# Kernel tuning notes

Measured on AMD Instinct MI355X. Metric: run time of the kernel, lower is better.

## Reference

```python
import jax, jax.numpy as jnp
import numpy as np

H, N_PATCH, F, DIM = 12, 196, 8, 768
DH = DIM // H            # 64
D3 = 3 * DH              # per-head dim after 3*dim projection = 192
SCALE = float(np.sqrt(DH) * H)
B, S = 8, 1 + N_PATCH * F  # 1569


def setup_inputs() -> dict:
    key = jax.random.key(0)
    ks = jax.random.split(key, 12)
    w = lambda k, shp: (jax.random.normal(k, shp, dtype=jnp.float32) * 0.02)
    return {
        "x": jax.random.normal(ks[0], (B, S, DIM), dtype=jnp.float32),
        "Wq": w(ks[1], (DIM, 3 * DIM)), "bq": jnp.zeros((3 * DIM,), jnp.float32),
        "Wk": w(ks[2], (DIM, 3 * DIM)), "bk": jnp.zeros((3 * DIM,), jnp.float32),
        "Wv": w(ks[3], (DIM, 3 * DIM)), "bv": jnp.zeros((3 * DIM,), jnp.float32),
        "Wt": w(ks[4], (3 * DIM, DIM)), "bt": jnp.zeros((DIM,), jnp.float32),
        "Wf": w(ks[5], (3 * DIM, DIM)), "bf": jnp.zeros((DIM,), jnp.float32),
    }


def _heads(t):
    # [b, s, 3*dim] -> [b, H, s, D3]
    b, s, _ = t.shape
    return t.reshape(b, s, H, D3).transpose(0, 2, 1, 3)


def _merge(t):
    # [b, H, s, D3] -> [b, s, 3*dim]
    b, _, s, _ = t.shape
    return t.transpose(0, 2, 1, 3).reshape(b, s, H * D3)


def _attn(q, k, v):
    a = jax.nn.softmax(jnp.einsum('bhqd,bhkd->bhqk', q, k) / SCALE, axis=-1)
    return jnp.einsum('bhqk,bhkd->bhqd', a, v)


def reference(x, Wq, bq, Wk, bk, Wv, bv, Wt, bt, Wf, bf):
    patches = x[:, 1:, :]                       # [b, n*F, dim]
    # NOTE: faithful to original code: v_mat comes from self.k, k_mat from self.v
    qm = _heads(patches @ Wq + bq)
    vm = _heads(patches @ Wk + bk)
    km = _heads(patches @ Wv + bv)

    # CLS attention over full sequence (here v from self.v, k from self.k)
    q_cls = _heads(x[:, 0:1, :] @ Wq + bq)      # [b,H,1,D3]
    v_cls = _heads(x @ Wv + bv)
    k_cls = _heads(x @ Wk + bk)
    inter_cls = _attn(q_cls, k_cls, v_cls)      # [b,H,1,D3]

    # Stage 1: temporal attention per patch (patches 1..n-1), vectorized.
    # tokens are frame-major: index = frame*n + patch, so slice p::n == patch p across frames
    def per_patch(t):
        b = t.shape[0]
        return t.reshape(b, H, F, N_PATCH, D3)[:, :, :, 1:, :].transpose(0, 1, 3, 2, 4)  # [b,H,n-1,F,D3]
    q5, k5, v5 = per_patch(qm), per_patch(km), per_patch(vm)
    a1 = jax.nn.softmax(jnp.einsum('bhpfd,bhpgd->bhpfg', q5, k5) / SCALE, axis=-1)
    t1 = jnp.einsum('bhpfg,bhpgd->bhpfd', a1, v5).sum(axis=3)   # [b,H,n-1,D3]
    t1 = jnp.tile(t1, (1, 1, F, 1))                              # [b,H,(n-1)*F,D3]
    ti = _merge(t1) @ Wt + bt                                    # [b,(n-1)*F,dim]

    # Stage 2 (same qkv swap as stage 1)
    q2 = _heads(ti @ Wq + bq)
    v2 = _heads(ti @ Wk + bk)
    k2 = _heads(ti @ Wv + bv)
    outs = [_attn(q2[:, :, 0:N_PATCH], k2[:, :, 0:N_PATCH], v2[:, :, 0:N_PATCH]).sum(axis=2, keepdims=True)]
    for xi in range(1, F):  # small fixed loop over num_frames
        o = _attn(q2[:, :, xi:xi + N_PATCH], k2[:, :, xi::N_PATCH], v2[:, :, xi::N_PATCH])
        outs.append(o.sum(axis=2, keepdims=True))
    t2 = jnp.concatenate(outs, axis=2)                           # [b,H,F,D3]
    t2 = jnp.tile(t2, (1, 1, N_PATCH, 1))                        # [b,H,F*n,D3]

    full = jnp.concatenate([inter_cls, t2], axis=2)              # [b,H,1+n*F,D3]
    return _merge(full) @ Wf + bf                                # [b,S,dim]
```

## Files before the change

kernel.cpp:

```cpp
#include <hip/hip_runtime.h>
#include <math.h>

#define B_    8
#define SEQ   1569
#define DIMX  768
#define H_    12
#define D3    192
#define F_    8
#define NP    196
#define P1    195
#define NCOL  2304
#define NS    6912
#define RSCALE (1.0f/96.0f)
#define NCHUNK 16
#define CH     99
#define CLS_STRIDE 196

typedef __bf16 bf16_t;
typedef bf16_t bf16x8 __attribute__((ext_vector_type(8)));
typedef float  f32x4  __attribute__((ext_vector_type(4)));

__device__ __forceinline__ void load_lds16(const bf16_t* g, bf16_t* l) {
  __builtin_amdgcn_global_load_lds(
      (const __attribute__((address_space(1))) void*)g,
      (__attribute__((address_space(3))) void*)l, 16, 0, 0);
}

__device__ __forceinline__ float block_max256(float v, float* red) {
  #pragma unroll
  for (int o = 32; o > 0; o >>= 1) v = fmaxf(v, __shfl_xor(v, o, 64));
  __syncthreads();
  if ((threadIdx.x & 63) == 0) red[threadIdx.x >> 6] = v;
  __syncthreads();
  return fmaxf(fmaxf(red[0], red[1]), fmaxf(red[2], red[3]));
}

__device__ __forceinline__ float block_sum256(float v, float* red) {
  #pragma unroll
  for (int o = 32; o > 0; o >>= 1) v += __shfl_xor(v, o, 64);
  __syncthreads();
  if ((threadIdx.x & 63) == 0) red[threadIdx.x >> 6] = v;
  __syncthreads();
  return red[0] + red[1] + red[2] + red[3];
}

__global__ __launch_bounds__(256) void cast_f32_bf16(
    const float* __restrict__ in, bf16_t* __restrict__ out, int n4) {
  const int i = blockIdx.x * 256 + threadIdx.x;
  if (i >= n4) return;
  const float4 v = ((const float4*)in)[i];
  bf16_t o4[4] = {(bf16_t)v.x, (bf16_t)v.y, (bf16_t)v.z, (bf16_t)v.w};
  ((uint2*)out)[i] = *(uint2*)o4;
}

__global__ __launch_bounds__(256) void concat_bias_kernel(
    const float* __restrict__ bq, const float* __restrict__ bk,
    const float* __restrict__ bv, float* __restrict__ qkvb) {
  const int i = blockIdx.x * 256 + threadIdx.x;
  if (i >= NS) return;
  float v;
  if (i < NCOL) v = bq[i];
  else if (i < 2 * NCOL) v = bk[i - NCOL];
  else v = bv[i - 2 * NCOL];
  qkvb[i] = v;
}

__global__ __launch_bounds__(256) void transpose_cast(
    const float* __restrict__ W, bf16_t* __restrict__ WT, int Kd, int Nd) {
  __shared__ float t[32][33];
  const int bn = blockIdx.x * 32;
  const int bk = blockIdx.y * 32;
  const int tx = threadIdx.x & 31, ty = threadIdx.x >> 5;
  #pragma unroll
  for (int i = 0; i < 32; i += 8)
    t[ty + i][tx] = W[(size_t)(bk + ty + i) * Nd + bn + tx];
  __syncthreads();
  #pragma unroll
  for (int i = 0; i < 32; i += 8)
    WT[(size_t)(bn + ty + i) * Kd + bk + tx] = (bf16_t)t[tx][ty + i];
}

__global__ __launch_bounds__(256) void gemm_mfma_bt(
    const bf16_t* __restrict__ A, const bf16_t* __restrict__ BT,
    const float* __restrict__ bias, void* __restrict__ C,
    int M, int N, int K, int MT, int NT, int GROUPM, int outBf16) {
  __shared__ bf16_t As[128 * 32];
  __shared__ bf16_t Bs[128 * 32];
  const int tid  = threadIdx.x;
  const int wave = tid >> 6, lane = tid & 63;

  const int pid   = blockIdx.x;
  const int npg   = GROUPM * NT;
  const int group = pid / npg;
  const int first_m = group * GROUPM;
  int gsm = MT - first_m; if (gsm > GROUPM) gsm = GROUPM;
  const int lpid  = pid % npg;
  const int m_tile = first_m + lpid % gsm;
  const int n_tile = lpid / gsm;
  const int row0 = m_tile * 128, col0 = n_tile * 128;

  const int fr = lane & 15, kg = lane >> 4;
  int ra0 = row0 + wave * 32 + fr;
  int ra1 = ra0 + 16;
  if (ra0 >= M) ra0 = M - 1;
  if (ra1 >= M) ra1 = M - 1;
  const bf16_t* Ap0 = A + (size_t)ra0 * K + kg * 8;
  const bf16_t* Ap1 = A + (size_t)ra1 * K + kg * 8;
  const bf16_t* Bp0 = BT + (size_t)(col0 + wave * 32 + fr) * K + kg * 8;
  const bf16_t* Bp1 = Bp0 + (size_t)16 * K;
  bf16_t* lA0 = &As[(wave * 2 + 0) * 512];
  bf16_t* lA1 = &As[(wave * 2 + 1) * 512];
  bf16_t* lB0 = &Bs[(wave * 2 + 0) * 512];
  bf16_t* lB1 = &Bs[(wave * 2 + 1) * 512];

  const int m0 = (wave & 1) * 64, n0 = (wave >> 1) * 64;
  const int mb = (wave & 1) * 4,  nb = (wave >> 1) * 4;
  f32x4 acc[4][4] = {};

  for (int k0 = 0; k0 < K; k0 += 32) {
    load_lds16(Ap0 + k0, lA0);
    load_lds16(Ap1 + k0, lA1);
    load_lds16(Bp0 + k0, lB0);
    load_lds16(Bp1 + k0, lB1);
    __syncthreads();

    bf16x8 af[4], bfr[4];
    #pragma unroll
    for (int i = 0; i < 4; ++i) {
      af[i]  = *(const bf16x8*)&As[(mb + i) * 512 + lane * 8];
      bfr[i] = *(const bf16x8*)&Bs[(nb + i) * 512 + lane * 8];
    }
    #pragma unroll
    for (int i = 0; i < 4; ++i)
      #pragma unroll
      for (int j = 0; j < 4; ++j)
        acc[i][j] = __builtin_amdgcn_mfma_f32_16x16x32_bf16(
            af[i], bfr[j], acc[i][j], 0, 0, 0);
    __syncthreads();
  }

  const int cc = lane & 15, cr4 = (lane >> 4) * 4;
  #pragma unroll
  for (int i = 0; i < 4; ++i) {
    #pragma unroll
    for (int j = 0; j < 4; ++j) {
      const int col = col0 + n0 + j * 16 + cc;
      const float bcol = bias[col];
      #pragma unroll
      for (int reg = 0; reg < 4; ++reg) {
        const int r = row0 + m0 + i * 16 + cr4 + reg;
        if (r < M) {
          const float v = acc[i][j][reg] + bcol;
          if (outBf16) ((bf16_t*)C)[(size_t)r * N + col] = (bf16_t)v;
          else         ((float*)C)[(size_t)r * N + col] = v;
        }
      }
    }
  }
}

__global__ __launch_bounds__(256) void xi0_scores_mfma(
    const bf16_t* __restrict__ QKV2, float* __restrict__ Smat) {
  __shared__ bf16_t As[128 * 32];
  __shared__ bf16_t Bs[128 * 32];
  const int tid  = threadIdx.x;
  const int wave = tid >> 6, lane = tid & 63;
  const int row0 = blockIdx.x * 128, col0 = blockIdx.y * 128;
  const int bh = blockIdx.z;
  const int b = bh / H_, h = bh % H_;
  const bf16_t* Abase = QKV2 + (size_t)b * P1 * NS + h * D3;
  const bf16_t* Bbase = QKV2 + (size_t)b * P1 * NS + 2 * NCOL + h * D3;

  const int fr = lane & 15, kg = lane >> 4;
  int ra0 = row0 + wave * 32 + fr;
  int ra1 = ra0 + 16;
  if (ra0 >= P1) ra0 = P1 - 1;
  if (ra1 >= P1) ra1 = P1 - 1;
  int cb0 = col0 + wave * 32 + fr;
  int cb1 = cb0 + 16;
  if (cb0 >= P1) cb0 = P1 - 1;
  if (cb1 >= P1) cb1 = P1 - 1;
  const bf16_t* Ap0 = Abase + (size_t)ra0 * NS + kg * 8;
  const bf16_t* Ap1 = Abase + (size_t)ra1 * NS + kg * 8;
  const bf16_t* Bp0 = Bbase + (size_t)cb0 * NS + kg * 8;
  const bf16_t* Bp1 = Bbase + (size_t)cb1 * NS + kg * 8;
  bf16_t* lA0 = &As[(wave * 2 + 0) * 512];
  bf16_t* lA1 = &As[(wave * 2 + 1) * 512];
  bf16_t* lB0 = &Bs[(wave * 2 + 0) * 512];
  bf16_t* lB1 = &Bs[(wave * 2 + 1) * 512];

  const int m0 = (wave & 1) * 64, n0 = (wave >> 1) * 64;
  const int mb = (wave & 1) * 4,  nb = (wave >> 1) * 4;
  f32x4 acc[4][4] = {};

  for (int k0 = 0; k0 < D3; k0 += 32) {
    load_lds16(Ap0 + k0, lA0);
    load_lds16(Ap1 + k0, lA1);
    load_lds16(Bp0 + k0, lB0);
    load_lds16(Bp1 + k0, lB1);
    __syncthreads();
    bf16x8 af[4], bfr[4];
    #pragma unroll
    for (int i = 0; i < 4; ++i) {
      af[i]  = *(const bf16x8*)&As[(mb + i) * 512 + lane * 8];
      bfr[i] = *(const bf16x8*)&Bs[(nb + i) * 512 + lane * 8];
    }
    #pragma unroll
    for (int i = 0; i < 4; ++i)
      #pragma unroll
      for (int j = 0; j < 4; ++j)
        acc[i][j] = __builtin_amdgcn_mfma_f32_16x16x32_bf16(
            af[i], bfr[j], acc[i][j], 0, 0, 0);
    __syncthreads();
  }

  float* S = Smat + (size_t)bh * P1 * P1;
  const int cc = lane & 15, cr4 = (lane >> 4) * 4;
  #pragma unroll
  for (int i = 0; i < 4; ++i)
    #pragma unroll
    for (int j = 0; j < 4; ++j) {
      const int col = col0 + n0 + j * 16 + cc;
      #pragma unroll
      for (int reg = 0; reg < 4; ++reg) {
        const int r = row0 + m0 + i * 16 + cr4 + reg;
        if (r < P1 && col < P1) S[(size_t)r * P1 + col] = acc[i][j][reg] * RSCALE;
      }
    }
}

__global__ __launch_bounds__(256) void xi0_finish_kernel(
    const float* __restrict__ Smat, const bf16_t* __restrict__ QKV2,
    bf16_t* __restrict__ FULL9b) {
  const int bh = blockIdx.x;
  const int b = bh / H_, h = bh % H_;
  __shared__ float mrow[P1], inv_l[P1], g[P1];
  const float* S = Smat + (size_t)bh * P1 * P1;
  const int tid = threadIdx.x;

  if (tid < P1) {
    float m = -1e30f;
    for (int k = 0; k < P1; ++k) m = fmaxf(m, S[(size_t)tid * P1 + k]);
    float l = 0.f;
    for (int k = 0; k < P1; ++k)
      l += expf(S[(size_t)tid * P1 + k] - m) * ((k == 0) ? 2.f : 1.f);
    mrow[tid] = m;
    inv_l[tid] = ((tid == 0) ? 2.f : 1.f) / l;
  }
  __syncthreads();
  if (tid < P1) {
    float s = 0.f;
    for (int r = 0; r < P1; ++r)
      s += expf(S[(size_t)r * P1 + tid] - mrow[r]) * inv_l[r];
    g[tid] = s * ((tid == 0) ? 2.f : 1.f);
  }
  __syncthreads();
  if (tid < D3) {
    float acc = 0.f;
    const bf16_t* vbase = QKV2 + (size_t)b * P1 * NS + NCOL + h * D3 + tid;
    for (int k = 0; k < P1; ++k)
      acc = fmaf(g[k], (float)vbase[(size_t)k * NS], acc);
    FULL9b[((size_t)b * 9 + 1) * NCOL + h * D3 + tid] = (bf16_t)acc;
  }
}

__global__ __launch_bounds__(256) void cls_part_kernel(
    const bf16_t* __restrict__ XQKV, float* __restrict__ CLSP, int b0) {
  const int h  = blockIdx.x % H_;
  const int bl = blockIdx.x / H_;
  const int b  = b0 + bl;
  const int c  = blockIdx.y;
  const int t0 = c * CH;
  const int tend = (t0 + CH < SEQ) ? t0 + CH : SEQ;
  __shared__ float qs[D3];
  __shared__ float sc[CH];
  __shared__ float red[4];
  const int tid = threadIdx.x;

  const bf16_t* Qr = XQKV + (size_t)bl * SEQ * NS + h * D3;
  if (tid < 24) {
    const bf16x8 q8 = *(const bf16x8*)(Qr + tid * 8);
    #pragma unroll
    for (int m2 = 0; m2 < 8; ++m2) qs[tid * 8 + m2] = (float)q8[m2];
  }
  __syncthreads();

  float lmax = -1e30f;
  for (int t = t0 + tid; t < tend; t += 256) {
    const bf16_t* kr = XQKV + ((size_t)bl * SEQ + t) * NS + NCOL + h * D3;
    float acc = 0.f;
    #pragma unroll 3
    for (int d = 0; d < D3; d += 8) {
      const bf16x8 k8 = *(const bf16x8*)(kr + d);
      #pragma unroll
      for (int m2 = 0; m2 < 8; ++m2) acc = fmaf(qs[d + m2], (float)k8[m2], acc);
    }
    acc *= RSCALE;
    sc[t - t0] = acc;
    lmax = fmaxf(lmax, acc);
  }
  const float m = block_max256(lmax, red);
  float lsum = 0.f;
  for (int t = t0 + tid; t < tend; t += 256) {
    const float e = expf(sc[t - t0] - m);
    sc[t - t0] = e;
    lsum += e;
  }
  const float L = block_sum256(lsum, red);
  __syncthreads();

  float* P = CLSP + ((size_t)(b * H_ + h) * NCHUNK + c) * CLS_STRIDE;
  if (tid < D3) {
    float acc = 0.f;
    const bf16_t* vbase = XQKV + ((size_t)bl * SEQ + t0) * NS + 2 * NCOL + h * D3 + tid;
    for (int t = t0; t < tend; ++t)
      acc = fmaf(sc[t - t0], (float)vbase[(size_t)(t - t0) * NS], acc);
    P[tid] = acc;
  }
  if (tid == 192) P[192] = m;
  if (tid == 193) P[193] = L;
}

__global__ __launch_bounds__(256) void cls_combine_kernel(
    const float* __restrict__ CLSP, bf16_t* __restrict__ FULL9b) {
  const int bh = blockIdx.x;
  const int tid = threadIdx.x;
  const float* P = CLSP + (size_t)bh * NCHUNK * CLS_STRIDE;

  float M = -1e30f;
  #pragma unroll
  for (int c = 0; c < NCHUNK; ++c) M = fmaxf(M, P[c * CLS_STRIDE + 192]);
  float L = 0.f;
  float w[NCHUNK];
  #pragma unroll
  for (int c = 0; c < NCHUNK; ++c) {
    w[c] = expf(P[c * CLS_STRIDE + 192] - M);
    L += P[c * CLS_STRIDE + 193] * w[c];
  }
  if (tid < D3) {
    float acc = 0.f;
    #pragma unroll
    for (int c = 0; c < NCHUNK; ++c)
      acc = fmaf(w[c], P[c * CLS_STRIDE + tid], acc);
    const int b = bh / H_, h = bh % H_;
    FULL9b[((size_t)b * 9 + 0) * NCOL + h * D3 + tid] = (bf16_t)(acc / L);
  }
}

__global__ __launch_bounds__(64) void temporal_kernel(
    const bf16_t* __restrict__ XQKV, bf16_t* __restrict__ T1U, int b0) {
  const int id = blockIdx.x;
  const int pi = id % P1;
  const int h  = (id / P1) % H_;
  const int bl = id / (P1 * H_);
  const int b  = b0 + bl;
  __shared__ float qs[8][196], ks[8][196];
  const int tid = threadIdx.x;

  #pragma unroll
  for (int i = 0; i < 6; ++i) {
    const int idx = tid + 64 * i;
    const int arr = idx / 192;
    const int c = idx % 192;
    const int f = c / 24, d0 = (c % 24) * 8;
    const size_t base = ((size_t)bl * SEQ + (size_t)f * NP + pi + 2) * NS +
                        (arr ? 2 * NCOL : 0) + h * D3 + d0;
    const bf16x8 v8 = *(const bf16x8*)(XQKV + base);
    float* dst = arr ? &ks[f][d0] : &qs[f][d0];
    #pragma unroll
    for (int m2 = 0; m2 < 8; ++m2) dst[m2] = (float)v8[m2];
  }
  __syncthreads();

  const int f = tid >> 3, g = tid & 7;
  float s = 0.f;
  for (int d = 0; d < D3; d += 4) {
    const float4 a4 = *(const float4*)&qs[f][d];
    const float4 b4 = *(const float4*)&ks[g][d];
    s = fmaf(a4.x, b4.x, s); s = fmaf(a4.y, b4.y, s);
    s = fmaf(a4.z, b4.z, s); s = fmaf(a4.w, b4.w, s);
  }
  s *= RSCALE;

  float m = s;
  #pragma unroll
  for (int o = 1; o < 8; o <<= 1) m = fmaxf(m, __shfl_xor(m, o, 64));
  const float e = expf(s - m);
  float sum = e;
  #pragma unroll
  for (int o = 1; o < 8; o <<= 1) sum += __shfl_xor(sum, o, 64);
  float a = e / sum;
  #pragma unroll
  for (int o = 8; o < 64; o <<= 1) a += __shfl_xor(a, o, 64);
  float wg[8];
  #pragma unroll
  for (int gg = 0; gg < 8; ++gg) wg[gg] = __shfl(a, gg, 64);

  const size_t vrow = (size_t)bl * SEQ * NS + NCOL + h * D3;
  #pragma unroll
  for (int i = 0; i < 3; ++i) {
    const int d = tid + 64 * i;
    float o = 0.f;
    #pragma unroll
    for (int gg = 0; gg < 8; ++gg) {
      const bf16_t vv = XQKV[vrow + ((size_t)gg * NP + pi + 2) * NS + d];
      o = fmaf(wg[gg], (float)vv, o);
    }
    T1U[((size_t)b * P1 + pi) * NCOL + h * D3 + d] = (bf16_t)o;
  }
}

__global__ __launch_bounds__(256) void stage2_xi_kernel(
    const bf16_t* __restrict__ QKV2, bf16_t* __restrict__ FULL9b) {
  const int xi = 1 + blockIdx.x % 7;
  const int h  = (blockIdx.x / 7) % H_;
  const int b  = blockIdx.x / (7 * H_);
  __shared__ float Ks[8][196], Vs[8][196], Qs[32][196];
  __shared__ float Pp[32][8];
  const int tid = threadIdx.x;

  for (int idx = tid; idx < 192; idx += 256) {
    const int k = idx / 24, d0 = (idx % 24) * 8;
    const bf16x8 v8 = *(const bf16x8*)(QKV2 + ((size_t)(b * P1 + xi + k)) * NS +
                                       2 * NCOL + h * D3 + d0);
    #pragma unroll
    for (int m2 = 0; m2 < 8; ++m2) Ks[k][d0 + m2] = (float)v8[m2];
  }
  for (int idx = tid; idx < 192; idx += 256) {
    const int k = idx / 24, d0 = (idx % 24) * 8;
    const bf16x8 v8 = *(const bf16x8*)(QKV2 + ((size_t)(b * P1 + xi + k)) * NS +
                                       NCOL + h * D3 + d0);
    #pragma unroll
    for (int m2 = 0; m2 < 8; ++m2) Vs[k][d0 + m2] = (float)v8[m2];
  }

  float acc = 0.f;
  for (int c = 0; c < 7; ++c) {
    __syncthreads();
    for (int idx = tid; idx < 768; idx += 256) {
      const int qr = idx / 24, d0 = (idx % 24) * 8;
      const int rq = c * 32 + qr;
      if (rq < P1) {
        const bf16x8 v8 = *(const bf16x8*)(QKV2 + ((size_t)(b * P1 + rq)) * NS +
                                           h * D3 + d0);
        #pragma unroll
        for (int m2 = 0; m2 < 8; ++m2) Qs[qr][d0 + m2] = (float)v8[m2];
      } else {
        #pragma unroll
        for (int m2 = 0; m2 < 8; ++m2) Qs[qr][d0 + m2] = 0.f;
      }
    }
    __syncthreads();
    const int grp = tid >> 3, k = tid & 7;
    float dot = 0.f;
    for (int d = 0; d < D3; d += 4) {
      const float4 a4 = *(const float4*)&Qs[grp][d];
      const float4 b4 = *(const float4*)&Ks[k][d];
      dot = fmaf(a4.x, b4.x, dot); dot = fmaf(a4.y, b4.y, dot);
      dot = fmaf(a4.z, b4.z, dot); dot = fmaf(a4.w, b4.w, dot);
    }
    dot *= RSCALE;
    float m = dot;
    #pragma unroll
    for (int o = 1; o < 8; o <<= 1) m = fmaxf(m, __shfl_xor(m, o, 64));
    const float e = expf(dot - m);
    float s = e;
    #pragma unroll
    for (int o = 1; o < 8; o <<= 1) s += __shfl_xor(s, o, 64);
    Pp[grp][k] = e / s;
    __syncthreads();
    if (tid < D3) {
      #pragma unroll 4
      for (int g2 = 0; g2 < 32; ++g2) {
        const int rq2 = c * 32 + g2;
        if (rq2 < P1) {
          const float mult = (rq2 == xi) ? 2.f : 1.f;
          float o = 0.f;
          #pragma unroll
          for (int kk = 0; kk < 8; ++kk) o = fmaf(Pp[g2][kk], Vs[kk][tid], o);
          acc = fmaf(mult, o, acc);
        }
      }
    }
  }
  if (tid < D3)
    FULL9b[((size_t)b * 9 + 1 + xi) * NCOL + h * D3 + tid] = (bf16_t)acc;
}

__global__ __launch_bounds__(256) void bcast_kernel(
    const float* __restrict__ OUT9, float* __restrict__ out) {
  const int idx = blockIdx.x * 256 + threadIdx.x;
  const int total = B_ * SEQ * (DIMX / 4);
  if (idx >= total) return;
  const int d4 = idx % (DIMX / 4);
  const int bs = idx / (DIMX / 4);
  const int s = bs % SEQ;
  const int b = bs / SEQ;
  const int row = (s == 0) ? 0 : 1 + ((s - 1) & 7);
  ((float4*)out)[idx] = ((const float4*)OUT9)[(size_t)(b * 9 + row) * (DIMX / 4) + d4];
}

extern "C" void kernel_launch(void* const* d_in, const int* in_sizes, int n_in,
                              void* d_out, int out_size, void* d_ws, size_t ws_size,
                              hipStream_t stream) {
  const float* x  = (const float*)d_in[0];
  const float* Wq = (const float*)d_in[1];
  const float* bq = (const float*)d_in[2];
  const float* Wk = (const float*)d_in[3];
  const float* bk = (const float*)d_in[4];
  const float* Wv = (const float*)d_in[5];
  const float* bv = (const float*)d_in[6];
  const float* Wt = (const float*)d_in[7];
  const float* bt = (const float*)d_in[8];
  const float* Wf = (const float*)d_in[9];
  const float* bf = (const float*)d_in[10];
  float* out = (float*)d_out;
  (void)in_sizes; (void)n_in; (void)out_size;

  char* ws = (char*)d_ws;
  size_t off = 0;
  auto alloc_f32 = [&](size_t elems) {
    size_t a = (off + 63) & ~(size_t)63;
    off = a + elems * sizeof(float);
    return (float*)(ws + a);
  };
  auto alloc_bf16 = [&](size_t elems) {
    size_t a = (off + 63) & ~(size_t)63;
    off = a + elems * sizeof(bf16_t);
    return (bf16_t*)(ws + a);
  };

  bf16_t* T1Ub   = alloc_bf16((size_t)B_ * P1 * NCOL);
  bf16_t* TIUb   = alloc_bf16((size_t)B_ * P1 * DIMX);
  bf16_t* QKV2b  = alloc_bf16((size_t)B_ * P1 * NS);
  bf16_t* FULL9b = alloc_bf16((size_t)B_ * 9 * NCOL);
  float*  OUT9   = alloc_f32((size_t)B_ * 9 * DIMX);
  float*  Smat   = alloc_f32((size_t)B_ * H_ * P1 * P1);
  float*  CLSP   = alloc_f32((size_t)B_ * H_ * NCHUNK * CLS_STRIDE);
  float*  QKVbias= alloc_f32(NS);
  bf16_t* WqkvT  = alloc_bf16((size_t)3 * NCOL * DIMX);
  bf16_t* WtT    = alloc_bf16((size_t)DIMX * NCOL);
  bf16_t* WfT    = alloc_bf16((size_t)DIMX * NCOL);

  const size_t remain = (ws_size > off) ? (ws_size - off) : 0;
  int Bc = 8;
  while (Bc > 1 &&
         (size_t)Bc * SEQ * (NS + DIMX) * sizeof(bf16_t) + 512 > remain)
    Bc >>= 1;
  bf16_t* XQKVb = alloc_bf16((size_t)Bc * SEQ * NS);
  bf16_t* xb    = alloc_bf16((size_t)Bc * SEQ * DIMX);

  transpose_cast<<<dim3(NCOL / 32, DIMX / 32), 256, 0, stream>>>(
      Wq, WqkvT + 0 * (size_t)NCOL * DIMX, DIMX, NCOL);
  transpose_cast<<<dim3(NCOL / 32, DIMX / 32), 256, 0, stream>>>(
      Wk, WqkvT + 1 * (size_t)NCOL * DIMX, DIMX, NCOL);
  transpose_cast<<<dim3(NCOL / 32, DIMX / 32), 256, 0, stream>>>(
      Wv, WqkvT + 2 * (size_t)NCOL * DIMX, DIMX, NCOL);
  transpose_cast<<<dim3(DIMX / 32, NCOL / 32), 256, 0, stream>>>(Wt, WtT, NCOL, DIMX);
  transpose_cast<<<dim3(DIMX / 32, NCOL / 32), 256, 0, stream>>>(Wf, WfT, NCOL, DIMX);
  concat_bias_kernel<<<dim3((NS + 255) / 256), 256, 0, stream>>>(bq, bk, bv, QKVbias);

  for (int b0 = 0; b0 < B_; b0 += Bc) {
    const int Mrows = Bc * SEQ;
    const int n4 = Mrows * DIMX / 4;
    cast_f32_bf16<<<dim3((n4 + 255) / 256), 256, 0, stream>>>(
        x + (size_t)b0 * SEQ * DIMX, xb, n4);
    const int MT = (Mrows + 127) / 128, NT = NS / 128;
    gemm_mfma_bt<<<dim3(MT * NT), 256, 0, stream>>>(
        xb, WqkvT, QKVbias, XQKVb, Mrows, NS, DIMX, MT, NT, 8, 1);
    cls_part_kernel<<<dim3(Bc * H_, NCHUNK), 256, 0, stream>>>(XQKVb, CLSP, b0);
    temporal_kernel<<<dim3(Bc * P1 * H_), 64, 0, stream>>>(XQKVb, T1Ub, b0);
  }
  cls_combine_kernel<<<dim3(B_ * H_), 256, 0, stream>>>(CLSP, FULL9b);

  {
    const int MT = (B_ * P1 + 127) / 128, NT = DIMX / 128;
    gemm_mfma_bt<<<dim3(MT * NT), 256, 0, stream>>>(
        T1Ub, WtT, bt, TIUb, B_ * P1, DIMX, NCOL, MT, NT, 4, 1);
  }
  {
    const int MT = (B_ * P1 + 127) / 128, NT = NS / 128;
    gemm_mfma_bt<<<dim3(MT * NT), 256, 0, stream>>>(
        TIUb, WqkvT, QKVbias, QKV2b, B_ * P1, NS, DIMX, MT, NT, 4, 1);
  }

  xi0_scores_mfma<<<dim3(2, 2, B_ * H_), 256, 0, stream>>>(QKV2b, Smat);
  xi0_finish_kernel<<<dim3(B_ * H_), 256, 0, stream>>>(Smat, QKV2b, FULL9b);
  stage2_xi_kernel<<<dim3(B_ * H_ * 7), 256, 0, stream>>>(QKV2b, FULL9b);

  {
    const int MT = 1, NT = DIMX / 128;
    gemm_mfma_bt<<<dim3(MT * NT), 256, 0, stream>>>(
        FULL9b, WfT, bf, OUT9, B_ * 9, DIMX, NCOL, MT, NT, 1, 0);
  }

  {
    const int total4 = B_ * SEQ * (DIMX / 4);
    bcast_kernel<<<dim3((total4 + 255) / 256), 256, 0, stream>>>(OUT9, out);
  }
}
```

Baseline: 834.7 us.

## Double-buffer GEMM LDS, XCD-aware tile mapping, batch temporal blocks, fuse weight transposes

The GEMM now double-buffers its A/B LDS tiles and prefetches the next K slice before computing the current one, using explicit waitcnt and barriers in place of full syncthreads. The big QKV GEMM gets an XCD-aware block-to-tile mapping so each of the 8 XCDs works on a contiguous band of M tiles, aiming at better L2 reuse. The temporal kernel packs four patches into one 256-thread block instead of one patch per 64-thread block. The five weight transpose launches are merged into one kernel. Risks are hand-coded waitcnt encodings being wrong for the target, LDS use doubling and lowering occupancy, and some wasted idle blocks in the XCD mapping.

```diff
diff --git a/kernel.cpp b/kernel.cpp
--- a/kernel.cpp
+++ b/kernel.cpp
@@ -15,6 +15,7 @@
 #define NCHUNK 16
 #define CH     99
 #define CLS_STRIDE 196
+#define PG4   49
 
 typedef __bf16 bf16_t;
 typedef bf16_t bf16x8 __attribute__((ext_vector_type(8)));
@@ -65,11 +66,27 @@
   qkvb[i] = v;
 }
 
-__global__ __launch_bounds__(256) void transpose_cast(
-    const float* __restrict__ W, bf16_t* __restrict__ WT, int Kd, int Nd) {
+__global__ __launch_bounds__(256) void transpose_all(
+    const float* __restrict__ Wq, const float* __restrict__ Wk,
+    const float* __restrict__ Wv, const float* __restrict__ Wt,
+    const float* __restrict__ Wf, bf16_t* __restrict__ WqkvT,
+    bf16_t* __restrict__ WtT, bf16_t* __restrict__ WfT) {
   __shared__ float t[32][33];
-  const int bn = blockIdx.x * 32;
-  const int bk = blockIdx.y * 32;
+  const int bid = blockIdx.x;
+  const int mat = bid / 1728, tt = bid % 1728;
+  const float* W; bf16_t* WT; int Kd, Nd, nt, kt;
+  if (mat < 3) {
+    Kd = DIMX; Nd = NCOL;
+    W = (mat == 0) ? Wq : ((mat == 1) ? Wk : Wv);
+    WT = WqkvT + (size_t)mat * NCOL * DIMX;
+    nt = tt % 72; kt = tt / 72;
+  } else {
+    Kd = NCOL; Nd = DIMX;
+    W = (mat == 3) ? Wt : Wf;
+    WT = (mat == 3) ? WtT : WfT;
+    nt = tt % 24; kt = tt / 24;
+  }
+  const int bn = nt * 32, bk = kt * 32;
   const int tx = threadIdx.x & 31, ty = threadIdx.x >> 5;
   #pragma unroll
   for (int i = 0; i < 32; i += 8)
@@ -83,20 +100,28 @@
 __global__ __launch_bounds__(256) void gemm_mfma_bt(
     const bf16_t* __restrict__ A, const bf16_t* __restrict__ BT,
     const float* __restrict__ bias, void* __restrict__ C,
-    int M, int N, int K, int MT, int NT, int GROUPM, int outBf16) {
-  __shared__ bf16_t As[128 * 32];
-  __shared__ bf16_t Bs[128 * 32];
+    int M, int N, int K, int MT, int NT, int GROUPM, int XCDB, int outBf16) {
+  __shared__ bf16_t As[2][128 * 32];
+  __shared__ bf16_t Bs[2][128 * 32];
   const int tid  = threadIdx.x;
   const int wave = tid >> 6, lane = tid & 63;
 
-  const int pid   = blockIdx.x;
-  const int npg   = GROUPM * NT;
-  const int group = pid / npg;
-  const int first_m = group * GROUPM;
-  int gsm = MT - first_m; if (gsm > GROUPM) gsm = GROUPM;
-  const int lpid  = pid % npg;
-  const int m_tile = first_m + lpid % gsm;
-  const int n_tile = lpid / gsm;
+  int m_tile, n_tile;
+  const int pid = blockIdx.x;
+  if (XCDB > 0) {
+    const int xcd = pid & 7, q = pid >> 3;
+    m_tile = xcd * XCDB + q % XCDB;
+    n_tile = q / XCDB;
+    if (m_tile >= MT) return;
+  } else {
+    const int npg   = GROUPM * NT;
+    const int group = pid / npg;
+    const int first_m = group * GROUPM;
+    int gsm = MT - first_m; if (gsm > GROUPM) gsm = GROUPM;
+    const int lpid  = pid % npg;
+    m_tile = first_m + lpid % gsm;
+    n_tile = lpid / gsm;
+  }
   const int row0 = m_tile * 128, col0 = n_tile * 128;
 
   const int fr = lane & 15, kg = lane >> 4;
@@ -108,27 +133,37 @@
   const bf16_t* Ap1 = A + (size_t)ra1 * K + kg * 8;
   const bf16_t* Bp0 = BT + (size_t)(col0 + wave * 32 + fr) * K + kg * 8;
   const bf16_t* Bp1 = Bp0 + (size_t)16 * K;
-  bf16_t* lA0 = &As[(wave * 2 + 0) * 512];
-  bf16_t* lA1 = &As[(wave * 2 + 1) * 512];
-  bf16_t* lB0 = &Bs[(wave * 2 + 0) * 512];
-  bf16_t* lB1 = &Bs[(wave * 2 + 1) * 512];
+  const int la0 = (wave * 2 + 0) * 512, la1 = (wave * 2 + 1) * 512;
 
   const int m0 = (wave & 1) * 64, n0 = (wave >> 1) * 64;
   const int mb = (wave & 1) * 4,  nb = (wave >> 1) * 4;
   f32x4 acc[4][4] = {};
 
-  for (int k0 = 0; k0 < K; k0 += 32) {
-    load_lds16(Ap0 + k0, lA0);
-    load_lds16(Ap1 + k0, lA1);
-    load_lds16(Bp0 + k0, lB0);
-    load_lds16(Bp1 + k0, lB1);
-    __syncthreads();
+  const int nk = K >> 5;
+  load_lds16(Ap0, &As[0][la0]);
+  load_lds16(Ap1, &As[0][la1]);
+  load_lds16(Bp0, &Bs[0][la0]);
+  load_lds16(Bp1, &Bs[0][la1]);
+
+  for (int kk = 0; kk < nk; ++kk) {
+    const int p = kk & 1;
+    if (kk + 1 < nk) {
+      const int k0 = (kk + 1) * 32;
+      load_lds16(Ap0 + k0, &As[p ^ 1][la0]);
+      load_lds16(Ap1 + k0, &As[p ^ 1][la1]);
+      load_lds16(Bp0 + k0, &Bs[p ^ 1][la0]);
+      load_lds16(Bp1 + k0, &Bs[p ^ 1][la1]);
+      __builtin_amdgcn_s_waitcnt(0x0F74);
+    } else {
+      __builtin_amdgcn_s_waitcnt(0x0F70);
+    }
+    __builtin_amdgcn_s_barrier();
 
     bf16x8 af[4], bfr[4];
     #pragma unroll
     for (int i = 0; i < 4; ++i) {
-      af[i]  = *(const bf16x8*)&As[(mb + i) * 512 + lane * 8];
-      bfr[i] = *(const bf16x8*)&Bs[(nb + i) * 512 + lane * 8];
+      af[i]  = *(const bf16x8*)&As[p][(mb + i) * 512 + lane * 8];
+      bfr[i] = *(const bf16x8*)&Bs[p][(nb + i) * 512 + lane * 8];
     }
     #pragma unroll
     for (int i = 0; i < 4; ++i)
@@ -136,7 +171,7 @@
       for (int j = 0; j < 4; ++j)
         acc[i][j] = __builtin_amdgcn_mfma_f32_16x16x32_bf16(
             af[i], bfr[j], acc[i][j], 0, 0, 0);
-    __syncthreads();
+    __builtin_amdgcn_s_barrier();
   }
 
   const int cc = lane & 15, cr4 = (lane >> 4) * 4;
@@ -347,36 +382,40 @@
   }
 }
 
-__global__ __launch_bounds__(64) void temporal_kernel(
+__global__ __launch_bounds__(256) void temporal_kernel(
     const bf16_t* __restrict__ XQKV, bf16_t* __restrict__ T1U, int b0) {
   const int id = blockIdx.x;
-  const int pi = id % P1;
-  const int h  = (id / P1) % H_;
-  const int bl = id / (P1 * H_);
+  const int pg = id % PG4;
+  const int h  = (id / PG4) % H_;
+  const int bl = id / (PG4 * H_);
   const int b  = b0 + bl;
-  __shared__ float qs[8][196], ks[8][196];
-  const int tid = threadIdx.x;
+  const int wave = threadIdx.x >> 6, lane = threadIdx.x & 63;
+  __shared__ float qs[4][8][196], ks[4][8][196];
+
+  int pi = pg * 4 + wave;
+  const bool act = (pi < P1);
+  if (!act) pi = P1 - 1;
 
   #pragma unroll
   for (int i = 0; i < 6; ++i) {
-    const int idx = tid + 64 * i;
+    const int idx = lane + 64 * i;
     const int arr = idx / 192;
     const int c = idx % 192;
     const int f = c / 24, d0 = (c % 24) * 8;
     const size_t base = ((size_t)bl * SEQ + (size_t)f * NP + pi + 2) * NS +
                         (arr ? 2 * NCOL : 0) + h * D3 + d0;
     const bf16x8 v8 = *(const bf16x8*)(XQKV + base);
-    float* dst = arr ? &ks[f][d0] : &qs[f][d0];
+    float* dst = arr ? &ks[wave][f][d0] : &qs[wave][f][d0];
     #pragma unroll
     for (int m2 = 0; m2 < 8; ++m2) dst[m2] = (float)v8[m2];
   }
   __syncthreads();
 
-  const int f = tid >> 3, g = tid & 7;
+  const int f = lane >> 3, g = lane & 7;
   float s = 0.f;
   for (int d = 0; d < D3; d += 4) {
-    const float4 a4 = *(const float4*)&qs[f][d];
-    const float4 b4 = *(const float4*)&ks[g][d];
+    const float4 a4 = *(const float4*)&qs[wave][f][d];
+    const float4 b4 = *(const float4*)&ks[wave][g][d];
     s = fmaf(a4.x, b4.x, s); s = fmaf(a4.y, b4.y, s);
     s = fmaf(a4.z, b4.z, s); s = fmaf(a4.w, b4.w, s);
   }
@@ -396,17 +435,19 @@
   #pragma unroll
   for (int gg = 0; gg < 8; ++gg) wg[gg] = __shfl(a, gg, 64);
 
-  const size_t vrow = (size_t)bl * SEQ * NS + NCOL + h * D3;
-  #pragma unroll
-  for (int i = 0; i < 3; ++i) {
-    const int d = tid + 64 * i;
-    float o = 0.f;
-    #pragma unroll
-    for (int gg = 0; gg < 8; ++gg) {
-      const bf16_t vv = XQKV[vrow + ((size_t)gg * NP + pi + 2) * NS + d];
-      o = fmaf(wg[gg], (float)vv, o);
-    }
-    T1U[((size_t)b * P1 + pi) * NCOL + h * D3 + d] = (bf16_t)o;
+  if (act) {
+    const size_t vrow = (size_t)bl * SEQ * NS + NCOL + h * D3;
+    #pragma unroll
+    for (int i = 0; i < 3; ++i) {
+      const int d = lane + 64 * i;
+      float o = 0.f;
+      #pragma unroll
+      for (int gg = 0; gg < 8; ++gg) {
+        const bf16_t vv = XQKV[vrow + ((size_t)gg * NP + pi + 2) * NS + d];
+        o = fmaf(wg[gg], (float)vv, o);
+      }
+      T1U[((size_t)b * P1 + pi) * NCOL + h * D3 + d] = (bf16_t)o;
+    }
   }
 }
 
@@ -550,14 +591,8 @@
   bf16_t* XQKVb = alloc_bf16((size_t)Bc * SEQ * NS);
   bf16_t* xb    = alloc_bf16((size_t)Bc * SEQ * DIMX);
 
-  transpose_cast<<<dim3(NCOL / 32, DIMX / 32), 256, 0, stream>>>(
-      Wq, WqkvT + 0 * (size_t)NCOL * DIMX, DIMX, NCOL);
-  transpose_cast<<<dim3(NCOL / 32, DIMX / 32), 256, 0, stream>>>(
-      Wk, WqkvT + 1 * (size_t)NCOL * DIMX, DIMX, NCOL);
-  transpose_cast<<<dim3(NCOL / 32, DIMX / 32), 256, 0, stream>>>(
-      Wv, WqkvT + 2 * (size_t)NCOL * DIMX, DIMX, NCOL);
-  transpose_cast<<<dim3(DIMX / 32, NCOL / 32), 256, 0, stream>>>(Wt, WtT, NCOL, DIMX);
-  transpose_cast<<<dim3(DIMX / 32, NCOL / 32), 256, 0, stream>>>(Wf, WfT, NCOL, DIMX);
+  transpose_all<<<dim3(1728 * 5), 256, 0, stream>>>(
+      Wq, Wk, Wv, Wt, Wf, WqkvT, WtT, WfT);
   concat_bias_kernel<<<dim3((NS + 255) / 256), 256, 0, stream>>>(bq, bk, bv, QKVbias);
 
   for (int b0 = 0; b0 < B_; b0 += Bc) {
@@ -566,22 +601,23 @@
     cast_f32_bf16<<<dim3((n4 + 255) / 256), 256, 0, stream>>>(
         x + (size_t)b0 * SEQ * DIMX, xb, n4);
     const int MT = (Mrows + 127) / 128, NT = NS / 128;
-    gemm_mfma_bt<<<dim3(MT * NT), 256, 0, stream>>>(
-        xb, WqkvT, QKVbias, XQKVb, Mrows, NS, DIMX, MT, NT, 8, 1);
+    const int XCDB = (MT + 7) / 8;
+    gemm_mfma_bt<<<dim3(8 * XCDB * NT), 256, 0, stream>>>(
+        xb, WqkvT, QKVbias, XQKVb, Mrows, NS, DIMX, MT, NT, 0, XCDB, 1);
     cls_part_kernel<<<dim3(Bc * H_, NCHUNK), 256, 0, stream>>>(XQKVb, CLSP, b0);
-    temporal_kernel<<<dim3(Bc * P1 * H_), 64, 0, stream>>>(XQKVb, T1Ub, b0);
+    temporal_kernel<<<dim3(Bc * H_ * PG4), 256, 0, stream>>>(XQKVb, T1Ub, b0);
   }
   cls_combine_kernel<<<dim3(B_ * H_), 256, 0, stream>>>(CLSP, FULL9b);
 
   {
     const int MT = (B_ * P1 + 127) / 128, NT = DIMX / 128;
     gemm_mfma_bt<<<dim3(MT * NT), 256, 0, stream>>>(
-        T1Ub, WtT, bt, TIUb, B_ * P1, DIMX, NCOL, MT, NT, 4, 1);
+        T1Ub, WtT, bt, TIUb, B_ * P1, DIMX, NCOL, MT, NT, 4, 0, 1);
   }
   {
     const int MT = (B_ * P1 + 127) / 128, NT = NS / 128;
     gemm_mfma_bt<<<dim3(MT * NT), 256, 0, stream>>>(
-        TIUb, WqkvT, QKVbias, QKV2b, B_ * P1, NS, DIMX, MT, NT, 4, 1);
+        TIUb, WqkvT, QKVbias, QKV2b, B_ * P1, NS, DIMX, MT, NT, 4, 0, 1);
   }
 
   xi0_scores_mfma<<<dim3(2, 2, B_ * H_), 256, 0, stream>>>(QKV2b, Smat);
@@ -591,7 +627,7 @@
   {
     const int MT = 1, NT = DIMX / 128;
     gemm_mfma_bt<<<dim3(MT * NT), 256, 0, stream>>>(
-        FULL9b, WfT, bf, OUT9, B_ * 9, DIMX, NCOL, MT, NT, 1, 0);
+        FULL9b, WfT, bf, OUT9, B_ * 9, DIMX, NCOL, MT, NT, 1, 0, 0);
   }
 
   {
```

Result: no change. 848.3 us (+1.6%).
